# Kernel optimization log

Measured on AMD Instinct MI355X. Metric: run time of the kernel, lower is better.

The kernel has to match this reference:

```python
import jax, jax.numpy as jnp
import numpy as np

B, D, C = 512, 512, 100000
U_M, L_M, U_A, L_A = 0.8, 0.45, 110.0, 10.0
LAMBDA_G, SCALE = 35.0, 64.0


def setup_inputs() -> dict:
    key = jax.random.key(0)
    k1, k2, k3, k4 = jax.random.split(key, 4)
    x = jax.random.normal(k1, (B, D), dtype=jnp.float32)
    # magnitudes in [l_a, u_a] as in MagFace
    x_norm = L_A + (U_A - L_A) * jax.random.uniform(k2, (B,), dtype=jnp.float32)
    labels = jax.random.randint(k3, (B,), 0, C, dtype=jnp.int64)
    weight = jax.random.normal(k4, (C, D), dtype=jnp.float32)
    return {"x": x, "x_norm": x_norm, "labels": labels, "weight": weight}


def _l2norm(a, axis=-1, eps=1e-12):
    return a / jnp.maximum(jnp.linalg.norm(a, axis=axis, keepdims=True), eps)


def reference(x, x_norm, labels, weight):
    # adaptive margin per sample, shape [B]
    margin = (U_M - L_M) / (U_A - L_A) * (x_norm - L_A) + L_M

    # cos_theta = normalize(x) @ normalize(W).T  -> [B, C]
    cos_theta = jnp.clip(_l2norm(x) @ _l2norm(weight).T, -1.0, 1.0)

    theta = jnp.arccos(cos_theta)
    valid = labels != -1  # [B]
    safe_labels = jnp.where(valid, labels, 0)
    # add margin at the target class (only for valid labels)
    add = jnp.where(valid, margin, 0.0)  # [B]
    theta = theta.at[jnp.arange(theta.shape[0]), safe_labels].add(add)

    logits = jnp.cos(theta) * SCALE  # [B, C]

    # cross-entropy, ignoring labels == -1
    lse = jax.nn.logsumexp(logits, axis=-1)  # [B]
    tgt = jnp.take_along_axis(logits, safe_labels[:, None], axis=-1)[:, 0]
    nll = jnp.where(valid, lse - tgt, 0.0)
    n_valid = jnp.maximum(jnp.sum(valid.astype(jnp.float32)), 1.0)
    ce = jnp.sum(nll) / n_valid

    # MagFace G-loss
    g_loss = jnp.mean(x_norm / (U_A * U_A) + 1.0 / x_norm)

    return ce + LAMBDA_G * g_loss
```

## Files before the change

kernel.cpp:

```cpp
#include <hip/hip_runtime.h>

typedef unsigned short u16;
typedef unsigned int u32;
typedef float f32x4 __attribute__((ext_vector_type(4)));
typedef short bf16x8 __attribute__((ext_vector_type(8)));

#define U_M 0.8f
#define L_M 0.45f
#define U_A 110.0f
#define L_A 10.0f
#define LAMBDA_G 35.0f
#define SCALEF 64.0f

__device__ __forceinline__ u16 f2bf(float f) {
  u32 u = __builtin_bit_cast(u32, f);
  u32 r = (u + 0x7fffu + ((u >> 16) & 1u)) >> 16;
  return (u16)r;
}

__device__ __forceinline__ u32 cvtpk(float lo, float hi) {
  u32 r;
  asm("v_cvt_pk_bf16_f32 %0, %1, %2" : "=v"(r) : "v"(lo), "v"(hi));
  return r;
}

__global__ void xnorm_kernel(const float* __restrict__ x, u16* __restrict__ xn, int K) {
  int row = blockIdx.x * 4 + (threadIdx.x >> 6);
  int l = threadIdx.x & 63;
  const float4* p = reinterpret_cast<const float4*>(x + (size_t)row * K) + l * 2;
  float4 a = p[0], b = p[1];
  float s = a.x*a.x + a.y*a.y + a.z*a.z + a.w*a.w
          + b.x*b.x + b.y*b.y + b.z*b.z + b.w*b.w;
  #pragma unroll
  for (int m = 32; m >= 1; m >>= 1) s += __shfl_xor(s, m);
  float inv = rsqrtf(fmaxf(s, 1e-24f));
  u32 q0 = (u32)f2bf(a.x*inv) | ((u32)f2bf(a.y*inv) << 16);
  u32 q1 = (u32)f2bf(a.z*inv) | ((u32)f2bf(a.w*inv) << 16);
  u32 q2 = (u32)f2bf(b.x*inv) | ((u32)f2bf(b.y*inv) << 16);
  u32 q3 = (u32)f2bf(b.z*inv) | ((u32)f2bf(b.w*inv) << 16);
  *reinterpret_cast<uint4*>(xn + (size_t)row * K + l * 8) = make_uint4(q0, q1, q2, q3);
}

__global__ void tgt_kernel(const float* __restrict__ x, const float* __restrict__ W,
                           const int* __restrict__ labels, float* __restrict__ tgtcos, int K) {
  int b = blockIdx.x;
  int l = threadIdx.x;
  int lab = labels[b];
  int labc = lab < 0 ? 0 : lab;
  const float4* px = reinterpret_cast<const float4*>(x + (size_t)b * K) + l * 2;
  const float4* pw = reinterpret_cast<const float4*>(W + (size_t)labc * K) + l * 2;
  float4 a0 = px[0], a1 = px[1], w0 = pw[0], w1 = pw[1];
  float dot = a0.x*w0.x + a0.y*w0.y + a0.z*w0.z + a0.w*w0.w
            + a1.x*w1.x + a1.y*w1.y + a1.z*w1.z + a1.w*w1.w;
  float sx = a0.x*a0.x + a0.y*a0.y + a0.z*a0.z + a0.w*a0.w
           + a1.x*a1.x + a1.y*a1.y + a1.z*a1.z + a1.w*a1.w;
  float sw = w0.x*w0.x + w0.y*w0.y + w0.z*w0.z + w0.w*w0.w
           + w1.x*w1.x + w1.y*w1.y + w1.z*w1.z + w1.w*w1.w;
  #pragma unroll
  for (int m = 32; m >= 1; m >>= 1) {
    dot += __shfl_xor(dot, m);
    sx  += __shfl_xor(sx, m);
    sw  += __shfl_xor(sw, m);
  }
  if (l == 0) {
    float cv = dot * rsqrtf(fmaxf(sx, 1e-24f)) * rsqrtf(fmaxf(sw, 1e-24f));
    tgtcos[b] = fminf(fmaxf(cv, -1.f), 1.f);
  }
}

__global__ __launch_bounds__(256, 2) void gemm_wf32(
    const u16* __restrict__ xn, const float* __restrict__ W,
    const int* __restrict__ labels,
    float* __restrict__ partials, int C, int K, int M) {
  __shared__ u16 sA[128 * 64];
  __shared__ u16 sB[128 * 64];
  __shared__ float bsum[2][128];
  __shared__ float sIw[128];
  __shared__ int slab[128];

  int nwg = gridDim.x;
  int id = blockIdx.x;
  int q = nwg >> 3, r = nwg & 7;
  int xcd = id & 7, pos = id >> 3;
  int wg = (xcd < r ? xcd * (q + 1) : r * (q + 1) + (xcd - r) * q) + pos;
  const int bm = wg & 3, bn = wg >> 2;

  const int t = threadIdx.x;
  const int l = t & 63, wid = t >> 6;
  const int wm = wid >> 1, wn_ = wid & 1;
  const int n0 = bn * 128;
  if (t < 128) slab[t] = labels[bm * 128 + t];

  const int qq = t & 3;
  const int rbase = t >> 2;
  float ssq0 = 0.f, ssq1 = 0.f;

  f32x4 acc[4][4] = {};
  const int nkt = K >> 6;
  for (int kt = 0; kt < nkt; ++kt) {
    const int k0 = kt << 6;

    float4 v0[4], v1[4];
    {
      int r0 = n0 + rbase;       r0 = r0 < C ? r0 : C - 1;
      int r1 = n0 + 64 + rbase;  r1 = r1 < C ? r1 : C - 1;
      const float4* p0 = reinterpret_cast<const float4*>(W + (size_t)r0 * K + k0 + qq * 16);
      const float4* p1 = reinterpret_cast<const float4*>(W + (size_t)r1 * K + k0 + qq * 16);
      #pragma unroll
      for (int j = 0; j < 4; ++j) v0[j] = p0[j];
      #pragma unroll
      for (int j = 0; j < 4; ++j) v1[j] = p1[j];
    }

    #pragma unroll
    for (int i = 0; i < 4; ++i) {
      int L = i * 256 + t;
      int rr = L >> 3;
      int cs = (L & 7) ^ (rr & 7);
      const u16* src = xn + (size_t)(bm * 128 + rr) * K + k0 + cs * 8;
      __builtin_amdgcn_global_load_lds(
          (const __attribute__((address_space(1))) void*)src,
          (__attribute__((address_space(3))) void*)(sA + (size_t)(i * 256 + (t & 192)) * 8),
          16, 0, 0);
    }

    #pragma unroll
    for (int pass = 0; pass < 2; ++pass) {
      const float4* v = pass ? v1 : v0;
      int rr = pass * 64 + rbase;
      float s = 0.f;
      u32 pk[8];
      #pragma unroll
      for (int j = 0; j < 4; ++j) {
        float4 f = v[j];
        s += f.x*f.x + f.y*f.y + f.z*f.z + f.w*f.w;
        pk[j*2]   = cvtpk(f.x, f.y);
        pk[j*2+1] = cvtpk(f.z, f.w);
      }
      if (pass) ssq1 += s; else ssq0 += s;
      int c0 = qq * 2;
      uint4 w0 = make_uint4(pk[0], pk[1], pk[2], pk[3]);
      uint4 w1 = make_uint4(pk[4], pk[5], pk[6], pk[7]);
      *reinterpret_cast<uint4*>(sB + rr * 64 + (((c0    ) ^ (rr & 7)) * 8)) = w0;
      *reinterpret_cast<uint4*>(sB + rr * 64 + (((c0 + 1) ^ (rr & 7)) * 8)) = w1;
    }

    __syncthreads();
    #pragma unroll
    for (int ks = 0; ks < 2; ++ks) {
      bf16x8 af[4], bfr[4];
      #pragma unroll
      for (int mi = 0; mi < 4; ++mi) {
        int row = wm * 64 + mi * 16 + (l & 15);
        int ch = ks * 4 + (l >> 4);
        af[mi] = *reinterpret_cast<const bf16x8*>(sA + row * 64 + ((ch ^ (row & 7)) * 8));
      }
      #pragma unroll
      for (int ni = 0; ni < 4; ++ni) {
        int row = wn_ * 64 + ni * 16 + (l & 15);
        int ch = ks * 4 + (l >> 4);
        bfr[ni] = *reinterpret_cast<const bf16x8*>(sB + row * 64 + ((ch ^ (row & 7)) * 8));
      }
      #pragma unroll
      for (int mi = 0; mi < 4; ++mi)
        #pragma unroll
        for (int ni = 0; ni < 4; ++ni)
          acc[mi][ni] = __builtin_amdgcn_mfma_f32_16x16x32_bf16(af[mi], bfr[ni], acc[mi][ni], 0, 0, 0);
    }
    __syncthreads();
  }

  {
    float s0 = ssq0 + __shfl_xor(ssq0, 1);
    s0 += __shfl_xor(s0, 2);
    float s1 = ssq1 + __shfl_xor(ssq1, 1);
    s1 += __shfl_xor(s1, 2);
    if (qq == 0) {
      sIw[rbase]      = rsqrtf(fmaxf(s0, 1e-24f));
      sIw[64 + rbase] = rsqrtf(fmaxf(s1, 1e-24f));
    }
  }
  __syncthreads();

  float iw[4]; int colv[4];
  #pragma unroll
  for (int ni = 0; ni < 4; ++ni) {
    int cl = wn_ * 64 + ni * 16 + (l & 15);
    colv[ni] = n0 + cl;
    iw[ni] = sIw[cl];
  }
  #pragma unroll
  for (int mi = 0; mi < 4; ++mi) {
    #pragma unroll
    for (int rg = 0; rg < 4; ++rg) {
      int row_l = wm * 64 + mi * 16 + ((l >> 4) << 2) + rg;
      int labr = slab[row_l];
      float rs = 0.f;
      #pragma unroll
      for (int ni = 0; ni < 4; ++ni) {
        float cv = acc[mi][ni][rg] * iw[ni];
        cv = fminf(fmaxf(cv, -1.f), 1.f);
        float e = __expf(SCALEF * cv - SCALEF);
        bool keep = (colv[ni] < C) && (colv[ni] != labr);
        rs += keep ? e : 0.f;
      }
      rs += __shfl_xor(rs, 1);
      rs += __shfl_xor(rs, 2);
      rs += __shfl_xor(rs, 4);
      rs += __shfl_xor(rs, 8);
      if ((l & 15) == 0) bsum[wn_][row_l] = rs;
    }
  }
  __syncthreads();
  if (t < 128) {
    partials[(size_t)bn * M + bm * 128 + t] = bsum[0][t] + bsum[1][t];
  }
}

__global__ void rowreduce_kernel(const float* __restrict__ partials, float* __restrict__ rowsum,
                                 int NBN, int M) {
  int b = blockIdx.x, t = threadIdx.x;
  float s = 0.f;
  for (int i = t; i < NBN; i += 256) s += partials[(size_t)i * M + b];
  __shared__ float sh[256];
  sh[t] = s; __syncthreads();
  for (int off = 128; off >= 1; off >>= 1) {
    if (t < off) sh[t] += sh[t + off];
    __syncthreads();
  }
  if (t == 0) rowsum[b] = sh[0];
}

__global__ void final_kernel(const float* __restrict__ rowsum, const float* __restrict__ tgtcos,
                             const float* __restrict__ x_norm, const int* __restrict__ labels,
                             float* __restrict__ out, int Bn) {
  int t = threadIdx.x;
  float nll = 0.f, g = 0.f, vld = 0.f;
  if (t < Bn) {
    float a = x_norm[t];
    g = a * (1.0f / (U_A * U_A)) + 1.0f / a;
    int lab = labels[t];
    bool valid = (lab != -1);
    if (valid) {
      float ct = tgtcos[t];
      float margin = ((U_M - L_M) / (U_A - L_A)) * (a - L_A) + L_M;
      float theta = acosf(ct) + margin;
      float tl = SCALEF * cosf(theta);
      float se = rowsum[t] + __expf(tl - SCALEF);
      float lse = SCALEF + logf(se);
      nll = lse - tl;
      vld = 1.f;
    }
  }
  __shared__ float s1[512], s2[512], s3[512];
  s1[t] = nll; s2[t] = g; s3[t] = vld;
  __syncthreads();
  for (int off = 256; off >= 1; off >>= 1) {
    if (t < off) { s1[t] += s1[t + off]; s2[t] += s2[t + off]; s3[t] += s3[t + off]; }
    __syncthreads();
  }
  if (t == 0) {
    float ce = s1[0] / fmaxf(s3[0], 1.f);
    out[0] = ce + LAMBDA_G * (s2[0] / (float)Bn);
  }
}

extern "C" void kernel_launch(void* const* d_in, const int* in_sizes, int n_in,
                              void* d_out, int out_size, void* d_ws, size_t ws_size,
                              hipStream_t stream) {
  const float* x      = (const float*)d_in[0];
  const float* x_norm = (const float*)d_in[1];
  const int*   labels = (const int*)d_in[2];
  const float* W      = (const float*)d_in[3];
  float* out = (float*)d_out;

  const int B = in_sizes[1];
  const int D = in_sizes[0] / B;
  const int C = in_sizes[3] / D;
  const int NBN = (C + 127) / 128;

  char* ws = (char*)d_ws;
  size_t o_xn   = 0;
  size_t o_tgt  = o_xn + (size_t)B * D * 2;
  size_t o_rows = o_tgt + (size_t)B * 4;
  size_t o_part = o_rows + (size_t)B * 4;

  u16*   xn       = (u16*)(ws + o_xn);
  float* tgtcos   = (float*)(ws + o_tgt);
  float* rowsum   = (float*)(ws + o_rows);
  float* partials = (float*)(ws + o_part);

  hipLaunchKernelGGL(xnorm_kernel, dim3(B / 4), dim3(256), 0, stream, x, xn, D);
  hipLaunchKernelGGL(tgt_kernel, dim3(B), dim3(64), 0, stream, x, W, labels, tgtcos, D);
  hipLaunchKernelGGL(gemm_wf32, dim3(NBN * (B / 128)), dim3(256), 0, stream,
                     xn, W, labels, partials, C, D, B);
  hipLaunchKernelGGL(rowreduce_kernel, dim3(B), dim3(256), 0, stream, partials, rowsum, NBN, B);
  hipLaunchKernelGGL(final_kernel, dim3(1), dim3(B), 0, stream, rowsum, tgtcos, x_norm, labels, out, B);
}
```

Measured before the change: 116.5 us.

## Double-buffer LDS tiles in the fused cosine GEMM to overlap loads with MFMA

Converts the GEMM main loop to a two-stage software pipeline with double-buffered LDS for the x and W tiles. The next K-tile's W fp32 loads and x async global-to-LDS copies are issued before the MFMAs on the current tile, and the bf16 conversion and store into the alternate buffer happen after them. This is meant to hide global memory latency behind compute and remove one barrier per iteration. The cost is double the LDS footprint (about 64KB) and extra live registers, which may put the 2-waves-per-SIMD occupancy target at risk.

```diff
diff --git a/kernel.cpp b/kernel.cpp
--- a/kernel.cpp
+++ b/kernel.cpp
@@ -68,12 +68,12 @@
   }
 }
 
-__global__ __launch_bounds__(256, 2) void gemm_wf32(
+__global__ __launch_bounds__(256, 2) void gemm_pipe(
     const u16* __restrict__ xn, const float* __restrict__ W,
     const int* __restrict__ labels,
     float* __restrict__ partials, int C, int K, int M) {
-  __shared__ u16 sA[128 * 64];
-  __shared__ u16 sB[128 * 64];
+  __shared__ u16 sA[2][128 * 64];
+  __shared__ u16 sB[2][128 * 64];
   __shared__ float bsum[2][128];
   __shared__ float sIw[128];
   __shared__ int slab[128];
@@ -86,44 +86,40 @@
   const int bm = wg & 3, bn = wg >> 2;
 
   const int t = threadIdx.x;
-  const int l = t & 63, wid = t >> 6;
-  const int wm = wid >> 1, wn_ = wid & 1;
+  const int l = t & 63;
+  const int wm = (t >> 6) >> 1, wn_ = (t >> 6) & 1;
   const int n0 = bn * 128;
   if (t < 128) slab[t] = labels[bm * 128 + t];
 
   const int qq = t & 3;
   const int rbase = t >> 2;
+  const int r0c = (n0 + rbase) < C ? (n0 + rbase) : C - 1;
+  const int r1c = (n0 + 64 + rbase) < C ? (n0 + 64 + rbase) : C - 1;
+  const float* wp0 = W + (size_t)r0c * K + qq * 16;
+  const float* wp1 = W + (size_t)r1c * K + qq * 16;
   float ssq0 = 0.f, ssq1 = 0.f;
 
-  f32x4 acc[4][4] = {};
   const int nkt = K >> 6;
-  for (int kt = 0; kt < nkt; ++kt) {
-    const int k0 = kt << 6;
-
-    float4 v0[4], v1[4];
-    {
-      int r0 = n0 + rbase;       r0 = r0 < C ? r0 : C - 1;
-      int r1 = n0 + 64 + rbase;  r1 = r1 < C ? r1 : C - 1;
-      const float4* p0 = reinterpret_cast<const float4*>(W + (size_t)r0 * K + k0 + qq * 16);
-      const float4* p1 = reinterpret_cast<const float4*>(W + (size_t)r1 * K + k0 + qq * 16);
-      #pragma unroll
-      for (int j = 0; j < 4; ++j) v0[j] = p0[j];
-      #pragma unroll
-      for (int j = 0; j < 4; ++j) v1[j] = p1[j];
-    }
-
+
+  float4 v0[4], v1[4];
+  {
+    const float4* p0 = reinterpret_cast<const float4*>(wp0);
+    const float4* p1 = reinterpret_cast<const float4*>(wp1);
+    #pragma unroll
+    for (int j = 0; j < 4; ++j) v0[j] = p0[j];
+    #pragma unroll
+    for (int j = 0; j < 4; ++j) v1[j] = p1[j];
     #pragma unroll
     for (int i = 0; i < 4; ++i) {
       int L = i * 256 + t;
       int rr = L >> 3;
       int cs = (L & 7) ^ (rr & 7);
-      const u16* src = xn + (size_t)(bm * 128 + rr) * K + k0 + cs * 8;
+      const u16* src = xn + (size_t)(bm * 128 + rr) * K + cs * 8;
       __builtin_amdgcn_global_load_lds(
           (const __attribute__((address_space(1))) void*)src,
-          (__attribute__((address_space(3))) void*)(sA + (size_t)(i * 256 + (t & 192)) * 8),
+          (__attribute__((address_space(3))) void*)(sA[0] + (size_t)(i * 256 + (t & 192)) * 8),
           16, 0, 0);
     }
-
     #pragma unroll
     for (int pass = 0; pass < 2; ++pass) {
       const float4* v = pass ? v1 : v0;
@@ -139,13 +135,42 @@
       }
       if (pass) ssq1 += s; else ssq0 += s;
       int c0 = qq * 2;
-      uint4 w0 = make_uint4(pk[0], pk[1], pk[2], pk[3]);
-      uint4 w1 = make_uint4(pk[4], pk[5], pk[6], pk[7]);
-      *reinterpret_cast<uint4*>(sB + rr * 64 + (((c0    ) ^ (rr & 7)) * 8)) = w0;
-      *reinterpret_cast<uint4*>(sB + rr * 64 + (((c0 + 1) ^ (rr & 7)) * 8)) = w1;
-    }
-
-    __syncthreads();
+      *reinterpret_cast<uint4*>(sB[0] + rr * 64 + (((c0    ) ^ (rr & 7)) * 8)) = make_uint4(pk[0], pk[1], pk[2], pk[3]);
+      *reinterpret_cast<uint4*>(sB[0] + rr * 64 + (((c0 + 1) ^ (rr & 7)) * 8)) = make_uint4(pk[4], pk[5], pk[6], pk[7]);
+    }
+  }
+  __syncthreads();
+
+  f32x4 acc[4][4] = {};
+  int cur = 0;
+  for (int kt = 0; kt < nkt; ++kt) {
+    const bool pf = (kt + 1) < nkt;
+    const u16* aCur = sA[cur];
+    const u16* bCur = sB[cur];
+    u16* aNxt = sA[cur ^ 1];
+    u16* bNxt = sB[cur ^ 1];
+
+    if (pf) {
+      const int k1 = (kt + 1) << 6;
+      const float4* p0 = reinterpret_cast<const float4*>(wp0 + k1);
+      const float4* p1 = reinterpret_cast<const float4*>(wp1 + k1);
+      #pragma unroll
+      for (int j = 0; j < 4; ++j) v0[j] = p0[j];
+      #pragma unroll
+      for (int j = 0; j < 4; ++j) v1[j] = p1[j];
+      #pragma unroll
+      for (int i = 0; i < 4; ++i) {
+        int L = i * 256 + t;
+        int rr = L >> 3;
+        int cs = (L & 7) ^ (rr & 7);
+        const u16* src = xn + (size_t)(bm * 128 + rr) * K + k1 + cs * 8;
+        __builtin_amdgcn_global_load_lds(
+            (const __attribute__((address_space(1))) void*)src,
+            (__attribute__((address_space(3))) void*)(aNxt + (size_t)(i * 256 + (t & 192)) * 8),
+            16, 0, 0);
+      }
+    }
+
     #pragma unroll
     for (int ks = 0; ks < 2; ++ks) {
       bf16x8 af[4], bfr[4];
@@ -153,13 +178,13 @@
       for (int mi = 0; mi < 4; ++mi) {
         int row = wm * 64 + mi * 16 + (l & 15);
         int ch = ks * 4 + (l >> 4);
-        af[mi] = *reinterpret_cast<const bf16x8*>(sA + row * 64 + ((ch ^ (row & 7)) * 8));
+        af[mi] = *reinterpret_cast<const bf16x8*>(aCur + row * 64 + ((ch ^ (row & 7)) * 8));
       }
       #pragma unroll
       for (int ni = 0; ni < 4; ++ni) {
         int row = wn_ * 64 + ni * 16 + (l & 15);
         int ch = ks * 4 + (l >> 4);
-        bfr[ni] = *reinterpret_cast<const bf16x8*>(sB + row * 64 + ((ch ^ (row & 7)) * 8));
+        bfr[ni] = *reinterpret_cast<const bf16x8*>(bCur + row * 64 + ((ch ^ (row & 7)) * 8));
       }
       #pragma unroll
       for (int mi = 0; mi < 4; ++mi)
@@ -167,7 +192,30 @@
         for (int ni = 0; ni < 4; ++ni)
           acc[mi][ni] = __builtin_amdgcn_mfma_f32_16x16x32_bf16(af[mi], bfr[ni], acc[mi][ni], 0, 0, 0);
     }
+
+    if (pf) {
+      #pragma unroll
+      for (int pass = 0; pass < 2; ++pass) {
+        const float4* v = pass ? v1 : v0;
+        int rr = pass * 64 + rbase;
+        float s = 0.f;
+        u32 pk[8];
+        #pragma unroll
+        for (int j = 0; j < 4; ++j) {
+          float4 f = v[j];
+          s += f.x*f.x + f.y*f.y + f.z*f.z + f.w*f.w;
+          pk[j*2]   = cvtpk(f.x, f.y);
+          pk[j*2+1] = cvtpk(f.z, f.w);
+        }
+        if (pass) ssq1 += s; else ssq0 += s;
+        int c0 = qq * 2;
+        *reinterpret_cast<uint4*>(bNxt + rr * 64 + (((c0    ) ^ (rr & 7)) * 8)) = make_uint4(pk[0], pk[1], pk[2], pk[3]);
+        *reinterpret_cast<uint4*>(bNxt + rr * 64 + (((c0 + 1) ^ (rr & 7)) * 8)) = make_uint4(pk[4], pk[5], pk[6], pk[7]);
+      }
+    }
+
     __syncthreads();
+    cur ^= 1;
   }
 
   {
@@ -292,7 +340,7 @@
 
   hipLaunchKernelGGL(xnorm_kernel, dim3(B / 4), dim3(256), 0, stream, x, xn, D);
   hipLaunchKernelGGL(tgt_kernel, dim3(B), dim3(64), 0, stream, x, W, labels, tgtcos, D);
-  hipLaunchKernelGGL(gemm_wf32, dim3(NBN * (B / 128)), dim3(256), 0, stream,
+  hipLaunchKernelGGL(gemm_pipe, dim3(NBN * (B / 128)), dim3(256), 0, stream,
                      xn, W, labels, partials, C, D, B);
   hipLaunchKernelGGL(rowreduce_kernel, dim3(B), dim3(256), 0, stream, partials, rowsum, NBN, B);
   hipLaunchKernelGGL(final_kernel, dim3(1), dim3(B), 0, stream, rowsum, tgtcos, x_norm, labels, out, B);
```

After: 166.6 us. +43.0%, slower.

## Double GEMM workgroup to 512 threads with 2x4 wave layout

Applied to the files above, without the earlier changes.

Doubles the GEMM workgroup from 256 to 512 threads, arranged as 2x4 waves, so each wave computes a 64x32 tile instead of 64x64. Each thread now loads and converts one W row segment per k-tile instead of two. The aim is more waves in flight to hide the fp32 W global loads and the bf16 conversion. The trade-off is fewer MFMAs per LDS fragment load and more waves contending at each barrier, with occupancy now set by launch_bounds(512,4).

```diff
diff --git a/kernel.cpp b/kernel.cpp
--- a/kernel.cpp
+++ b/kernel.cpp
@@ -68,13 +68,13 @@
   }
 }
 
-__global__ __launch_bounds__(256, 2) void gemm_wf32(
+__global__ __launch_bounds__(512, 4) void gemm_wf32(
     const u16* __restrict__ xn, const float* __restrict__ W,
     const int* __restrict__ labels,
     float* __restrict__ partials, int C, int K, int M) {
   __shared__ u16 sA[128 * 64];
   __shared__ u16 sB[128 * 64];
-  __shared__ float bsum[2][128];
+  __shared__ float bsum[4][128];
   __shared__ float sIw[128];
   __shared__ int slab[128];
 
@@ -87,47 +87,41 @@
 
   const int t = threadIdx.x;
   const int l = t & 63, wid = t >> 6;
-  const int wm = wid >> 1, wn_ = wid & 1;
+  const int wm = wid >> 2, wn_ = wid & 3;
   const int n0 = bn * 128;
   if (t < 128) slab[t] = labels[bm * 128 + t];
 
   const int qq = t & 3;
   const int rbase = t >> 2;
-  float ssq0 = 0.f, ssq1 = 0.f;
-
-  f32x4 acc[4][4] = {};
+  const int rc = (n0 + rbase) < C ? (n0 + rbase) : C - 1;
+  const float* wp = W + (size_t)rc * K + qq * 16;
+  float ssq = 0.f;
+
+  f32x4 acc[4][2] = {};
   const int nkt = K >> 6;
   for (int kt = 0; kt < nkt; ++kt) {
     const int k0 = kt << 6;
 
-    float4 v0[4], v1[4];
+    float4 v[4];
     {
-      int r0 = n0 + rbase;       r0 = r0 < C ? r0 : C - 1;
-      int r1 = n0 + 64 + rbase;  r1 = r1 < C ? r1 : C - 1;
-      const float4* p0 = reinterpret_cast<const float4*>(W + (size_t)r0 * K + k0 + qq * 16);
-      const float4* p1 = reinterpret_cast<const float4*>(W + (size_t)r1 * K + k0 + qq * 16);
-      #pragma unroll
-      for (int j = 0; j < 4; ++j) v0[j] = p0[j];
-      #pragma unroll
-      for (int j = 0; j < 4; ++j) v1[j] = p1[j];
+      const float4* p = reinterpret_cast<const float4*>(wp + k0);
+      #pragma unroll
+      for (int j = 0; j < 4; ++j) v[j] = p[j];
     }
 
     #pragma unroll
-    for (int i = 0; i < 4; ++i) {
-      int L = i * 256 + t;
+    for (int i = 0; i < 2; ++i) {
+      int L = i * 512 + t;
       int rr = L >> 3;
       int cs = (L & 7) ^ (rr & 7);
       const u16* src = xn + (size_t)(bm * 128 + rr) * K + k0 + cs * 8;
       __builtin_amdgcn_global_load_lds(
           (const __attribute__((address_space(1))) void*)src,
-          (__attribute__((address_space(3))) void*)(sA + (size_t)(i * 256 + (t & 192)) * 8),
+          (__attribute__((address_space(3))) void*)(sA + (size_t)(i * 512 + (t & 448)) * 8),
           16, 0, 0);
     }
 
-    #pragma unroll
-    for (int pass = 0; pass < 2; ++pass) {
-      const float4* v = pass ? v1 : v0;
-      int rr = pass * 64 + rbase;
+    {
       float s = 0.f;
       u32 pk[8];
       #pragma unroll
@@ -137,18 +131,16 @@
         pk[j*2]   = cvtpk(f.x, f.y);
         pk[j*2+1] = cvtpk(f.z, f.w);
       }
-      if (pass) ssq1 += s; else ssq0 += s;
+      ssq += s;
       int c0 = qq * 2;
-      uint4 w0 = make_uint4(pk[0], pk[1], pk[2], pk[3]);
-      uint4 w1 = make_uint4(pk[4], pk[5], pk[6], pk[7]);
-      *reinterpret_cast<uint4*>(sB + rr * 64 + (((c0    ) ^ (rr & 7)) * 8)) = w0;
-      *reinterpret_cast<uint4*>(sB + rr * 64 + (((c0 + 1) ^ (rr & 7)) * 8)) = w1;
+      *reinterpret_cast<uint4*>(sB + rbase * 64 + (((c0    ) ^ (rbase & 7)) * 8)) = make_uint4(pk[0], pk[1], pk[2], pk[3]);
+      *reinterpret_cast<uint4*>(sB + rbase * 64 + (((c0 + 1) ^ (rbase & 7)) * 8)) = make_uint4(pk[4], pk[5], pk[6], pk[7]);
     }
 
     __syncthreads();
     #pragma unroll
     for (int ks = 0; ks < 2; ++ks) {
-      bf16x8 af[4], bfr[4];
+      bf16x8 af[4], bfr[2];
       #pragma unroll
       for (int mi = 0; mi < 4; ++mi) {
         int row = wm * 64 + mi * 16 + (l & 15);
@@ -156,36 +148,31 @@
         af[mi] = *reinterpret_cast<const bf16x8*>(sA + row * 64 + ((ch ^ (row & 7)) * 8));
       }
       #pragma unroll
-      for (int ni = 0; ni < 4; ++ni) {
-        int row = wn_ * 64 + ni * 16 + (l & 15);
+      for (int ni = 0; ni < 2; ++ni) {
+        int row = wn_ * 32 + ni * 16 + (l & 15);
         int ch = ks * 4 + (l >> 4);
         bfr[ni] = *reinterpret_cast<const bf16x8*>(sB + row * 64 + ((ch ^ (row & 7)) * 8));
       }
       #pragma unroll
       for (int mi = 0; mi < 4; ++mi)
         #pragma unroll
-        for (int ni = 0; ni < 4; ++ni)
+        for (int ni = 0; ni < 2; ++ni)
           acc[mi][ni] = __builtin_amdgcn_mfma_f32_16x16x32_bf16(af[mi], bfr[ni], acc[mi][ni], 0, 0, 0);
     }
     __syncthreads();
   }
 
   {
-    float s0 = ssq0 + __shfl_xor(ssq0, 1);
+    float s0 = ssq + __shfl_xor(ssq, 1);
     s0 += __shfl_xor(s0, 2);
-    float s1 = ssq1 + __shfl_xor(ssq1, 1);
-    s1 += __shfl_xor(s1, 2);
-    if (qq == 0) {
-      sIw[rbase]      = rsqrtf(fmaxf(s0, 1e-24f));
-      sIw[64 + rbase] = rsqrtf(fmaxf(s1, 1e-24f));
-    }
+    if (qq == 0) sIw[rbase] = rsqrtf(fmaxf(s0, 1e-24f));
   }
   __syncthreads();
 
-  float iw[4]; int colv[4];
-  #pragma unroll
-  for (int ni = 0; ni < 4; ++ni) {
-    int cl = wn_ * 64 + ni * 16 + (l & 15);
+  float iw[2]; int colv[2];
+  #pragma unroll
+  for (int ni = 0; ni < 2; ++ni) {
+    int cl = wn_ * 32 + ni * 16 + (l & 15);
     colv[ni] = n0 + cl;
     iw[ni] = sIw[cl];
   }
@@ -197,7 +184,7 @@
       int labr = slab[row_l];
       float rs = 0.f;
       #pragma unroll
-      for (int ni = 0; ni < 4; ++ni) {
+      for (int ni = 0; ni < 2; ++ni) {
         float cv = acc[mi][ni][rg] * iw[ni];
         cv = fminf(fmaxf(cv, -1.f), 1.f);
         float e = __expf(SCALEF * cv - SCALEF);
@@ -213,7 +200,8 @@
   }
   __syncthreads();
   if (t < 128) {
-    partials[(size_t)bn * M + bm * 128 + t] = bsum[0][t] + bsum[1][t];
+    partials[(size_t)bn * M + bm * 128 + t] =
+        (bsum[0][t] + bsum[1][t]) + (bsum[2][t] + bsum[3][t]);
   }
 }
 
@@ -292,7 +280,7 @@
 
   hipLaunchKernelGGL(xnorm_kernel, dim3(B / 4), dim3(256), 0, stream, x, xn, D);
   hipLaunchKernelGGL(tgt_kernel, dim3(B), dim3(64), 0, stream, x, W, labels, tgtcos, D);
-  hipLaunchKernelGGL(gemm_wf32, dim3(NBN * (B / 128)), dim3(256), 0, stream,
+  hipLaunchKernelGGL(gemm_wf32, dim3(NBN * (B / 128)), dim3(512), 0, stream,
                      xn, W, labels, partials, C, D, B);
   hipLaunchKernelGGL(rowreduce_kernel, dim3(B), dim3(256), 0, stream, partials, rowsum, NBN, B);
   hipLaunchKernelGGL(final_kernel, dim3(1), dim3(B), 0, stream, rowsum, tgtcos, x_norm, labels, out, B);
```

Measured after the change: 129.9 us. 1.11x slower.

## Load fp32 weight tiles directly to LDS and convert to bf16 at fragment read

Applied to the files above, without the earlier changes.

The fp32 weight tile is now streamed into shared memory with asynchronous global_load_lds instead of going through registers with an explicit bf16 convert-and-store. The bf16 conversion and the weight row sum-of-squares move to the point where each wave reads its MFMA B fragments, and the row norms are reduced with lane shuffles afterwards. This removes the register staging and the LDS write pass for W. In exchange it doubles LDS usage for the B tile (32 KB fp32), which may limit occupancy. It also makes every wave repeat the conversion work, and W loads are no longer held in registers, so they cannot overlap with the MFMAs.

```diff
diff --git a/kernel.cpp b/kernel.cpp
--- a/kernel.cpp
+++ b/kernel.cpp
@@ -68,12 +68,12 @@
   }
 }
 
-__global__ __launch_bounds__(256, 2) void gemm_wf32(
+__global__ __launch_bounds__(256, 2) void gemm_gl(
     const u16* __restrict__ xn, const float* __restrict__ W,
     const int* __restrict__ labels,
     float* __restrict__ partials, int C, int K, int M) {
   __shared__ u16 sA[128 * 64];
-  __shared__ u16 sB[128 * 64];
+  __shared__ float sBf[128 * 64];
   __shared__ float bsum[2][128];
   __shared__ float sIw[128];
   __shared__ int slab[128];
@@ -91,26 +91,12 @@
   const int n0 = bn * 128;
   if (t < 128) slab[t] = labels[bm * 128 + t];
 
-  const int qq = t & 3;
-  const int rbase = t >> 2;
-  float ssq0 = 0.f, ssq1 = 0.f;
-
+  float ssq[4] = {0.f, 0.f, 0.f, 0.f};
   f32x4 acc[4][4] = {};
   const int nkt = K >> 6;
+
   for (int kt = 0; kt < nkt; ++kt) {
     const int k0 = kt << 6;
-
-    float4 v0[4], v1[4];
-    {
-      int r0 = n0 + rbase;       r0 = r0 < C ? r0 : C - 1;
-      int r1 = n0 + 64 + rbase;  r1 = r1 < C ? r1 : C - 1;
-      const float4* p0 = reinterpret_cast<const float4*>(W + (size_t)r0 * K + k0 + qq * 16);
-      const float4* p1 = reinterpret_cast<const float4*>(W + (size_t)r1 * K + k0 + qq * 16);
-      #pragma unroll
-      for (int j = 0; j < 4; ++j) v0[j] = p0[j];
-      #pragma unroll
-      for (int j = 0; j < 4; ++j) v1[j] = p1[j];
-    }
 
     #pragma unroll
     for (int i = 0; i < 4; ++i) {
@@ -123,29 +109,21 @@
           (__attribute__((address_space(3))) void*)(sA + (size_t)(i * 256 + (t & 192)) * 8),
           16, 0, 0);
     }
-
-    #pragma unroll
-    for (int pass = 0; pass < 2; ++pass) {
-      const float4* v = pass ? v1 : v0;
-      int rr = pass * 64 + rbase;
-      float s = 0.f;
-      u32 pk[8];
-      #pragma unroll
-      for (int j = 0; j < 4; ++j) {
-        float4 f = v[j];
-        s += f.x*f.x + f.y*f.y + f.z*f.z + f.w*f.w;
-        pk[j*2]   = cvtpk(f.x, f.y);
-        pk[j*2+1] = cvtpk(f.z, f.w);
-      }
-      if (pass) ssq1 += s; else ssq0 += s;
-      int c0 = qq * 2;
-      uint4 w0 = make_uint4(pk[0], pk[1], pk[2], pk[3]);
-      uint4 w1 = make_uint4(pk[4], pk[5], pk[6], pk[7]);
-      *reinterpret_cast<uint4*>(sB + rr * 64 + (((c0    ) ^ (rr & 7)) * 8)) = w0;
-      *reinterpret_cast<uint4*>(sB + rr * 64 + (((c0 + 1) ^ (rr & 7)) * 8)) = w1;
-    }
-
-    __syncthreads();
+    #pragma unroll
+    for (int j = 0; j < 8; ++j) {
+      int L = j * 256 + t;
+      int rr = L >> 4;
+      int cs = (L & 15) ^ (rr & 7);
+      int gr = n0 + rr; gr = gr < C ? gr : C - 1;
+      const float* src = W + (size_t)gr * K + k0 + cs * 4;
+      __builtin_amdgcn_global_load_lds(
+          (const __attribute__((address_space(1))) void*)src,
+          (__attribute__((address_space(3))) void*)(sBf + (size_t)(j * 256 + (t & 192)) * 4),
+          16, 0, 0);
+    }
+
+    __syncthreads();
+
     #pragma unroll
     for (int ks = 0; ks < 2; ++ks) {
       bf16x8 af[4], bfr[4];
@@ -159,7 +137,17 @@
       for (int ni = 0; ni < 4; ++ni) {
         int row = wn_ * 64 + ni * 16 + (l & 15);
         int ch = ks * 4 + (l >> 4);
-        bfr[ni] = *reinterpret_cast<const bf16x8*>(sB + row * 64 + ((ch ^ (row & 7)) * 8));
+        int c1 = (2 * ch)     ^ (row & 7);
+        int c2 = (2 * ch + 1) ^ (row & 7);
+        f32x4 fa = *reinterpret_cast<const f32x4*>(sBf + row * 64 + c1 * 4);
+        f32x4 fb = *reinterpret_cast<const f32x4*>(sBf + row * 64 + c2 * 4);
+        if (wm == 0) {
+          ssq[ni] += fa[0]*fa[0] + fa[1]*fa[1] + fa[2]*fa[2] + fa[3]*fa[3]
+                   + fb[0]*fb[0] + fb[1]*fb[1] + fb[2]*fb[2] + fb[3]*fb[3];
+        }
+        uint4 u = make_uint4(cvtpk(fa[0], fa[1]), cvtpk(fa[2], fa[3]),
+                             cvtpk(fb[0], fb[1]), cvtpk(fb[2], fb[3]));
+        bfr[ni] = __builtin_bit_cast(bf16x8, u);
       }
       #pragma unroll
       for (int mi = 0; mi < 4; ++mi)
@@ -170,14 +158,13 @@
     __syncthreads();
   }
 
-  {
-    float s0 = ssq0 + __shfl_xor(ssq0, 1);
-    s0 += __shfl_xor(s0, 2);
-    float s1 = ssq1 + __shfl_xor(ssq1, 1);
-    s1 += __shfl_xor(s1, 2);
-    if (qq == 0) {
-      sIw[rbase]      = rsqrtf(fmaxf(s0, 1e-24f));
-      sIw[64 + rbase] = rsqrtf(fmaxf(s1, 1e-24f));
+  if (wm == 0) {
+    #pragma unroll
+    for (int ni = 0; ni < 4; ++ni) {
+      float s = ssq[ni];
+      s += __shfl_xor(s, 16);
+      s += __shfl_xor(s, 32);
+      if ((l >> 4) == 0) sIw[wn_ * 64 + ni * 16 + l] = rsqrtf(fmaxf(s, 1e-24f));
     }
   }
   __syncthreads();
@@ -292,7 +279,7 @@
 
   hipLaunchKernelGGL(xnorm_kernel, dim3(B / 4), dim3(256), 0, stream, x, xn, D);
   hipLaunchKernelGGL(tgt_kernel, dim3(B), dim3(64), 0, stream, x, W, labels, tgtcos, D);
-  hipLaunchKernelGGL(gemm_wf32, dim3(NBN * (B / 128)), dim3(256), 0, stream,
+  hipLaunchKernelGGL(gemm_gl, dim3(NBN * (B / 128)), dim3(256), 0, stream,
                      xn, W, labels, partials, C, D, B);
   hipLaunchKernelGGL(rowreduce_kernel, dim3(B), dim3(256), 0, stream, partials, rowsum, NBN, B);
   hipLaunchKernelGGL(final_kernel, dim3(1), dim3(B), 0, stream, rowsum, tgtcos, x_norm, labels, out, B);
```

New measurement: 121.7 us. 1.04x slower.
